# Kernel tuning notes

Measured on AMD Instinct MI355X. Metric: run time of the kernel, lower is better.

Reference implementation:

```python
import jax, jax.numpy as jnp
import numpy as np
from jax import lax

V, E, H = 32000, 512, 512
B, S = 64, 64


def _lstm_cell(x, h, c, wih, whh, b):
    # PyTorch gate order: i, f, g, o
    g = x @ wih.T + h @ whh.T + b
    i, f, gg, o = jnp.split(g, 4, axis=-1)
    c2 = jax.nn.sigmoid(f) * c + jax.nn.sigmoid(i) * jnp.tanh(gg)
    h2 = jax.nn.sigmoid(o) * jnp.tanh(c2)
    return h2, c2


def setup_inputs() -> dict:
    key = jax.random.key(0)
    ks = jax.random.split(key, 16)
    s = 0.05
    return {
        "hidden_state": jax.random.normal(ks[0], (4, B, H), jnp.float32) * s,
        "cell_state": jax.random.normal(ks[1], (4, B, H), jnp.float32) * s,
        "Y": jax.random.randint(ks[2], (B, S), 0, V),
        "emb": jax.random.normal(ks[3], (V, E), jnp.float32) * s,
        "w_ih_l0": jax.random.normal(ks[4], (2, 4 * H, E), jnp.float32) * s,
        "w_hh_l0": jax.random.normal(ks[5], (2, 4 * H, H), jnp.float32) * s,
        "b_ih_l0": jax.random.normal(ks[6], (2, 4 * H), jnp.float32) * s,
        "b_hh_l0": jax.random.normal(ks[7], (2, 4 * H), jnp.float32) * s,
        "w_ih_l1": jax.random.normal(ks[8], (2, 4 * H, 2 * H), jnp.float32) * s,
        "w_hh_l1": jax.random.normal(ks[9], (2, 4 * H, H), jnp.float32) * s,
        "b_ih_l1": jax.random.normal(ks[10], (2, 4 * H), jnp.float32) * s,
        "b_hh_l1": jax.random.normal(ks[11], (2, 4 * H), jnp.float32) * s,
        "fc_w": jax.random.normal(ks[12], (V, 2 * H), jnp.float32) * s,
        "fc_b": jax.random.normal(ks[13], (V,), jnp.float32) * s,
    }


def reference(hidden_state, cell_state, Y, emb, w_ih_l0, w_hh_l0, b_ih_l0,
              b_hh_l0, w_ih_l1, w_hh_l1, b_ih_l1, b_hh_l1, fc_w, fc_b):
    # Deterministic teacher-forcing: input at step 0 is Y[:,1]; at step i>0 it is Y[:,i-1].
    idx_seq = jnp.concatenate([Y[:, 1:2], Y[:, :-1]], axis=1)  # (B,S)
    xs = idx_seq.T  # (S,B)
    b0 = b_ih_l0 + b_hh_l0  # (2,4H)
    b1 = b_ih_l1 + b_hh_l1

    def step(carry, idx):
        h, c = carry  # (4,B,H): [l0_fwd, l0_bwd, l1_fwd, l1_bwd]
        x = emb[idx]  # (B,E)
        h0f, c0f = _lstm_cell(x, h[0], c[0], w_ih_l0[0], w_hh_l0[0], b0[0])
        h0b, c0b = _lstm_cell(x, h[1], c[1], w_ih_l0[1], w_hh_l0[1], b0[1])
        x1 = jnp.concatenate([h0f, h0b], axis=-1)  # (B,2H)
        h1f, c1f = _lstm_cell(x1, h[2], c[2], w_ih_l1[0], w_hh_l1[0], b1[0])
        h1b, c1b = _lstm_cell(x1, h[3], c[3], w_ih_l1[1], w_hh_l1[1], b1[1])
        out = jnp.concatenate([h1f, h1b], axis=-1)  # (B,2H)
        h2 = jnp.stack([h0f, h0b, h1f, h1b])
        c2 = jnp.stack([c0f, c0b, c1f, c1b])
        return (h2, c2), out

    (_, _), outs = lax.scan(step, (hidden_state, cell_state), xs)  # (S,B,2H)
    logits = outs @ fc_w.T + fc_b  # (S,B,V)
    # permute to (B,S,V) then flatten, as in the torch code
    return jnp.transpose(logits, (1, 0, 2)).reshape(-1, fc_w.shape[0])
```

## Files before the change

### kernel.cpp

```cpp
#include <hip/hip_runtime.h>
#include <hip/hip_bf16.h>
#include <stdint.h>

#define S_ 64
#define B_ 64
#define E_ 512
#define H_ 512
#define V_ 32000
#define G4 2048
#define SB 4096
#define NG 4096

typedef __attribute__((ext_vector_type(8))) short short8;
typedef __attribute__((ext_vector_type(4))) float f32x4;
typedef __attribute__((ext_vector_type(4))) int i32x4;

static __device__ __forceinline__ unsigned short f2bf(float f) {
  unsigned u = __float_as_uint(f);
  u += 0x7fff + ((u >> 16) & 1);
  return (unsigned short)(u >> 16);
}
static __device__ __forceinline__ float sigm(float x) {
  return 1.f / (1.f + expf(-x));
}

__device__ __forceinline__ void gload_lds16(const void* g, void* l) {
  __builtin_amdgcn_global_load_lds(
      (const __attribute__((address_space(1))) void*)g,
      (__attribute__((address_space(3))) void*)l, 16, 0, 0);
}

__device__ __forceinline__ void st128_sys(void* p, i32x4 v) {
  asm volatile("global_store_dwordx4 %0, %1, off sc0 sc1"
               :: "v"((unsigned long long)p), "v"(v) : "memory");
}
__device__ __forceinline__ void wait_vm0() {
  asm volatile("s_waitcnt vmcnt(0)" ::: "memory");
}

__device__ __forceinline__ void spin_ge(unsigned* c, unsigned tgt) {
  while (__hip_atomic_load(c, __ATOMIC_RELAXED, __HIP_MEMORY_SCOPE_AGENT) < tgt)
    __builtin_amdgcn_s_sleep(1);
}
__device__ __forceinline__ void arrive(unsigned* c) {
  __hip_atomic_fetch_add(c, 1u, __ATOMIC_RELAXED, __HIP_MEMORY_SCOPE_AGENT);
}

#define CIDX(t, d, p) ((((t) * 8) + ((d) * 4) + (p)) * 64)
#define CNT_BYTES (64 * 8 * 64 * 4)

__global__ void k_f2bf(const float* __restrict__ in, unsigned short* __restrict__ out, int n) {
  int i = blockIdx.x * blockDim.x + threadIdx.x;
  int stride = gridDim.x * blockDim.x;
  for (; i < n; i += stride) out[i] = f2bf(in[i]);
}

__global__ void k_addbias(const float* __restrict__ a, const float* __restrict__ b,
                          float* __restrict__ out, int n) {
  int i = blockIdx.x * blockDim.x + threadIdx.x;
  if (i < n) out[i] = a[i] + b[i];
}

__global__ void k_gather(const int* __restrict__ Y, const float* __restrict__ emb,
                         unsigned short* __restrict__ X) {
  int sb = blockIdx.x;
  int t = sb >> 6, b = sb & 63;
  int idx = (t == 0) ? Y[b * S_ + 1] : Y[b * S_ + t - 1];
  const float* src = emb + (size_t)idx * E_;
  unsigned short* dst = X + (size_t)sb * E_;
  for (int e = threadIdx.x; e < E_; e += blockDim.x) dst[e] = f2bf(src[e]);
}

__global__ void k_init_h(const float* __restrict__ hid,
                         unsigned short* __restrict__ h0i, unsigned short* __restrict__ h1i) {
  int i = blockIdx.x * blockDim.x + threadIdx.x;
  if (i >= 4 * B_ * H_) return;
  unsigned short v = f2bf(hid[i]);
  if (i < 2 * B_ * H_) h0i[i] = v;
  else h1i[i - 2 * B_ * H_] = v;
}

template <bool PERMUTE, bool NT>
__global__ __launch_bounds__(256) void k_gemm_nt(
    const unsigned short* __restrict__ A, const unsigned short* __restrict__ B,
    const float* __restrict__ bias, float* __restrict__ C,
    int M, int N, int K, int nTM, int nwg) {
  __shared__ unsigned short Als[128 * 32];
  __shared__ unsigned short Bls[128 * 32];
  int tid = threadIdx.x;
  int o = blockIdx.x;
  int wg = (o & 7) * (nwg >> 3) + (o >> 3);
  int bm = wg % nTM, bn = wg / nTM;
  int w = tid >> 6, l = tid & 63;
  int wr = w >> 1, wc = w & 1;
  int lr = l & 15, hi = l >> 4;
  int c0 = w * 128 + l;
  int row0 = c0 >> 2, ks0 = (((c0 & 3) ^ (row0 & 3)) * 8);
  int c1 = c0 + 64;
  int row1 = c1 >> 2, ks1 = (((c1 & 3) ^ (row1 & 3)) * 8);
  const unsigned short* Ab = A + (size_t)(bm * 128) * K;
  const unsigned short* Bb = B + (size_t)(bn * 128) * K;
  unsigned short* AlsW = &Als[w * 1024];
  unsigned short* BlsW = &Bls[w * 1024];
  int co = ((hi ^ (lr & 3)) * 8);
  f32x4 acc[4][4] = {};
  for (int kk = 0; kk < K; kk += 32) {
    __syncthreads();
    gload_lds16(Ab + (size_t)row0 * K + kk + ks0, AlsW);
    gload_lds16(Ab + (size_t)row1 * K + kk + ks1, AlsW + 512);
    gload_lds16(Bb + (size_t)row0 * K + kk + ks0, BlsW);
    gload_lds16(Bb + (size_t)row1 * K + kk + ks1, BlsW + 512);
    __syncthreads();
    short8 af[4], bfr[4];
#pragma unroll
    for (int r = 0; r < 4; r++)
      af[r] = *(const short8*)&Als[(wr * 64 + r * 16 + lr) * 32 + co];
#pragma unroll
    for (int c4 = 0; c4 < 4; c4++)
      bfr[c4] = *(const short8*)&Bls[(wc * 64 + c4 * 16 + lr) * 32 + co];
#pragma unroll
    for (int r = 0; r < 4; r++)
#pragma unroll
      for (int c4 = 0; c4 < 4; c4++)
        acc[r][c4] = __builtin_amdgcn_mfma_f32_16x16x32_bf16(af[r], bfr[c4], acc[r][c4], 0, 0, 0);
  }
  int rbase = bm * 128 + wr * 64 + hi * 4;
  int cbase = bn * 128 + wc * 64 + lr;
#pragma unroll
  for (int r = 0; r < 4; r++) {
#pragma unroll
    for (int c4 = 0; c4 < 4; c4++) {
      int cc = cbase + c4 * 16;
      float bv = bias[cc];
#pragma unroll
      for (int j = 0; j < 4; j++) {
        int rr = rbase + r * 16 + j;
        size_t orow = PERMUTE ? (size_t)((rr & 63) * 64 + (rr >> 6)) : (size_t)rr;
        float v = acc[r][c4][j] + bv;
        float* p = &C[orow * (size_t)N + cc];
        if (NT) __builtin_nontemporal_store(v, p);
        else *p = v;
      }
    }
  }
}

#define LDW0 520
#define LDW1 1544
#define NBLK 192

__global__ __launch_bounds__(256) void k_fused_lstm(
    const unsigned short* __restrict__ h0i,
    const unsigned short* __restrict__ h1i,
    const float* __restrict__ cell,
    const unsigned short* __restrict__ whh0,
    const unsigned short* __restrict__ wih1,
    const unsigned short* __restrict__ whh1,
    const float* __restrict__ b1s,
    const float* __restrict__ G0,
    unsigned short* __restrict__ H0,
    unsigned short* __restrict__ O1,
    unsigned* __restrict__ cnt0, unsigned* __restrict__ cnt1) {
  __shared__ unsigned short SM[32 * LDW1];
  __shared__ __align__(16) unsigned short HS[64 * 16];
  int tid = threadIdx.x;
  int w = tid >> 6, l = tid & 63;
  int lr = l & 15, hi = l >> 4;

  if (blockIdx.x < 64) {
    int d = blockIdx.x >> 5, jt = blockIdx.x & 31;
    const unsigned short* Wd = whh0 + (size_t)d * (G4 * H_);
    for (int c = tid; c < 64 * 64; c += 256) {
      int row = c >> 6, ck = c & 63;
      int g = row >> 4, r16 = row & 15;
      *(int4*)&SM[row * LDW0 + ck * 8] =
          *(const int4*)&Wd[(size_t)(g * H_ + jt * 16 + r16) * H_ + ck * 8];
    }
    int j = jt * 16 + lr;
    int b0 = w * 16 + hi * 4;
    f32x4 creg;
    {
      const float* cd = cell + (size_t)d * (B_ * H_);
#pragma unroll
      for (int jj = 0; jj < 4; jj++) creg[jj] = cd[(size_t)(b0 + jj) * H_ + j];
    }
    __syncthreads();
    const float* G_dj = G0 + d * G4;
    float gv[4][4];
    auto preloadG = [&](int t) {
#pragma unroll
      for (int jj = 0; jj < 4; jj++) {
        const float* Gb = G_dj + (size_t)(t * B_ + b0 + jj) * NG;
#pragma unroll
        for (int g = 0; g < 4; g++) gv[g][jj] = Gb[g * 512 + j];
      }
    };
    preloadG(0);
    for (int t = 0; t < S_; ++t) {
      if (t >= 1) {
        if (tid < 4) spin_ge(&cnt0[CIDX(t - 1, d, tid)], 8);
        __syncthreads();
      }
      const unsigned short* hp = (t == 0) ? h0i + (size_t)d * (B_ * H_)
                                          : H0 + (size_t)(t - 1) * B_ * 1024 + d * 512;
      size_t hstr = (t == 0) ? (size_t)H_ : 1024;
      const unsigned short* arow = hp + (size_t)(w * 16 + lr) * hstr + hi * 8;
      f32x4 acc[4] = {};
#pragma unroll
      for (int ki = 0; ki < 16; ki++) {
        short8 a = *(const short8*)&arow[ki * 32];
#pragma unroll
        for (int g = 0; g < 4; g++) {
          short8 bfr = *(const short8*)&SM[(g * 16 + lr) * LDW0 + ki * 32 + hi * 8];
          acc[g] = __builtin_amdgcn_mfma_f32_16x16x32_bf16(a, bfr, acc[g], 0, 0, 0);
        }
      }
#pragma unroll
      for (int jj = 0; jj < 4; jj++) {
        float gi = acc[0][jj] + gv[0][jj];
        float gf = acc[1][jj] + gv[1][jj];
        float gg = acc[2][jj] + gv[2][jj];
        float go = acc[3][jj] + gv[3][jj];
        float c = sigm(gf) * creg[jj] + sigm(gi) * tanhf(gg);
        creg[jj] = c;
        HS[(b0 + jj) * 16 + lr] = f2bf(sigm(go) * tanhf(c));
      }
      __syncthreads();
      unsigned short* Ho = H0 + (size_t)t * B_ * 1024 + d * 512 + jt * 16;
      if (tid < 128) {
        int r = tid >> 1, half = tid & 1;
        i32x4 v = *(const i32x4*)&HS[r * 16 + half * 8];
        st128_sys(&Ho[(size_t)r * 1024 + half * 8], v);
      }
      wait_vm0();
      __syncthreads();
      if (tid == 0) arrive(&cnt0[CIDX(t, d, jt & 3)]);
      if (t + 1 < S_) preloadG(t + 1);
    }
  } else {
    int idx = blockIdx.x - 64;
    int d = idx >> 6, jt8 = idx & 63;
    int j0 = jt8 * 8;
    {
      const unsigned short* Wih = wih1 + (size_t)d * (G4 * 1024);
      const unsigned short* Whh = whh1 + (size_t)d * (G4 * H_);
      for (int c = tid; c < 32 * 192; c += 256) {
        int r = c / 192, ck = c - r * 192;
        int g = r >> 3, jc = r & 7;
        const unsigned short* src =
            (ck < 128) ? Wih + (size_t)(g * H_ + j0 + jc) * 1024 + ck * 8
                       : Whh + (size_t)(g * H_ + j0 + jc) * H_ + (ck - 128) * 8;
        *(int4*)&SM[r * LDW1 + ck * 8] = *(const int4*)src;
      }
    }
    int j = j0 + (lr & 7);
    const float* b1d = b1s + d * G4;
    float bi_ = b1d[j], bf_ = b1d[512 + j], bg_ = b1d[1024 + j], bo_ = b1d[1536 + j];
    int b0 = w * 16 + hi * 4;
    f32x4 creg = {};
    if (lr < 8) {
      const float* cd = cell + (size_t)(2 + d) * (B_ * H_);
#pragma unroll
      for (int jj = 0; jj < 4; jj++) creg[jj] = cd[(size_t)(b0 + jj) * H_ + j];
    }
    __syncthreads();

    f32x4 acc0, acc1;
    {
      if (tid < 8) spin_ge(&cnt0[CIDX(0, 0, 0) + tid * 64], 8);
      __syncthreads();
      acc0 = {}; acc1 = {};
      const unsigned short* x1row = H0 + ((size_t)0 * B_ + w * 16 + lr) * 1024 + hi * 8;
#pragma unroll 8
      for (int ki = 0; ki < 32; ki++) {
        short8 a = *(const short8*)&x1row[ki * 32];
        short8 bA = *(const short8*)&SM[(size_t)lr * LDW1 + ki * 32 + hi * 8];
        short8 bB = *(const short8*)&SM[(size_t)(16 + lr) * LDW1 + ki * 32 + hi * 8];
        acc0 = __builtin_amdgcn_mfma_f32_16x16x32_bf16(a, bA, acc0, 0, 0, 0);
        acc1 = __builtin_amdgcn_mfma_f32_16x16x32_bf16(a, bB, acc1, 0, 0, 0);
      }
    }
    for (int t = 0; t < S_; ++t) {
      if (t >= 1) {
        if (tid < 4) spin_ge(&cnt1[CIDX(t - 1, d, tid)], 16);
        __syncthreads();
      }
      const unsigned short* hprev = (t == 0)
          ? h1i + (size_t)d * (B_ * H_) + (size_t)(w * 16 + lr) * H_ + hi * 8
          : O1 + ((size_t)(t - 1) * B_ + w * 16 + lr) * 1024 + d * 512 + hi * 8;
#pragma unroll 8
      for (int ki = 0; ki < 16; ki++) {
        short8 a = *(const short8*)&hprev[ki * 32];
        short8 bA = *(const short8*)&SM[(size_t)lr * LDW1 + 1024 + ki * 32 + hi * 8];
        short8 bB = *(const short8*)&SM[(size_t)(16 + lr) * LDW1 + 1024 + ki * 32 + hi * 8];
        acc0 = __builtin_amdgcn_mfma_f32_16x16x32_bf16(a, bA, acc0, 0, 0, 0);
        acc1 = __builtin_amdgcn_mfma_f32_16x16x32_bf16(a, bB, acc1, 0, 0, 0);
      }
      float pf[4], po[4];
#pragma unroll
      for (int jj = 0; jj < 4; jj++) {
        pf[jj] = __shfl_xor(acc0[jj], 8);
        po[jj] = __shfl_xor(acc1[jj], 8);
      }
      if (lr < 8) {
#pragma unroll
        for (int jj = 0; jj < 4; jj++) {
          float gi = acc0[jj] + bi_;
          float gf = pf[jj] + bf_;
          float gg = acc1[jj] + bg_;
          float go = po[jj] + bo_;
          float c = sigm(gf) * creg[jj] + sigm(gi) * tanhf(gg);
          creg[jj] = c;
          HS[(b0 + jj) * 8 + lr] = f2bf(sigm(go) * tanhf(c));
        }
      }
      __syncthreads();
      unsigned short* Oo = O1 + (size_t)t * B_ * 1024 + d * 512 + j0;
      if (tid < 64) {
        i32x4 v = *(const i32x4*)&HS[tid * 8];
        st128_sys(&Oo[(size_t)tid * 1024], v);
      }
      wait_vm0();
      __syncthreads();
      if (tid == 0 && t + 1 < S_) arrive(&cnt1[CIDX(t, d, jt8 & 3)]);
      if (t + 1 < S_) {
        if (tid < 8) spin_ge(&cnt0[CIDX(t + 1, 0, 0) + tid * 64], 8);
        __syncthreads();
        acc0 = {}; acc1 = {};
        const unsigned short* x1row =
            H0 + ((size_t)(t + 1) * B_ + w * 16 + lr) * 1024 + hi * 8;
#pragma unroll 8
        for (int ki = 0; ki < 32; ki++) {
          short8 a = *(const short8*)&x1row[ki * 32];
          short8 bA = *(const short8*)&SM[(size_t)lr * LDW1 + ki * 32 + hi * 8];
          short8 bB = *(const short8*)&SM[(size_t)(16 + lr) * LDW1 + ki * 32 + hi * 8];
          acc0 = __builtin_amdgcn_mfma_f32_16x16x32_bf16(a, bA, acc0, 0, 0, 0);
          acc1 = __builtin_amdgcn_mfma_f32_16x16x32_bf16(a, bB, acc1, 0, 0, 0);
        }
      }
    }
  }
}

extern "C" void kernel_launch(void* const* d_in, const int* in_sizes, int n_in,
                              void* d_out, int out_size, void* d_ws, size_t ws_size,
                              hipStream_t stream) {
  const float* hidden = (const float*)d_in[0];
  const float* cell   = (const float*)d_in[1];
  const int*   Y      = (const int*)d_in[2];
  const float* emb    = (const float*)d_in[3];
  const float* wih0   = (const float*)d_in[4];
  const float* whh0   = (const float*)d_in[5];
  const float* bih0   = (const float*)d_in[6];
  const float* bhh0   = (const float*)d_in[7];
  const float* wih1   = (const float*)d_in[8];
  const float* whh1   = (const float*)d_in[9];
  const float* bih1   = (const float*)d_in[10];
  const float* bhh1   = (const float*)d_in[11];
  const float* fcw    = (const float*)d_in[12];
  const float* fcb    = (const float*)d_in[13];

  char* ws = (char*)d_ws;
  size_t off = 0;
  auto alloc = [&](size_t bytes) {
    void* p = ws + off;
    off += (bytes + 255) & ~(size_t)255;
    return p;
  };
  unsigned short* wih0b = (unsigned short*)alloc((size_t)2 * G4 * E_ * 2);
  unsigned short* whh0b = (unsigned short*)alloc((size_t)2 * G4 * H_ * 2);
  unsigned short* wih1b = (unsigned short*)alloc((size_t)2 * G4 * 1024 * 2);
  unsigned short* whh1b = (unsigned short*)alloc((size_t)2 * G4 * H_ * 2);
  unsigned short* fcwb  = (unsigned short*)alloc((size_t)V_ * 1024 * 2);
  unsigned short* Xb    = (unsigned short*)alloc((size_t)SB * E_ * 2);
  unsigned short* H0    = (unsigned short*)alloc((size_t)SB * 1024 * 2);
  unsigned short* O1    = (unsigned short*)alloc((size_t)SB * 1024 * 2);
  unsigned short* h0i   = (unsigned short*)alloc((size_t)2 * B_ * H_ * 2);
  unsigned short* h1i   = (unsigned short*)alloc((size_t)2 * B_ * H_ * 2);
  float* b0s = (float*)alloc((size_t)2 * G4 * 4);
  float* b1s = (float*)alloc((size_t)2 * G4 * 4);
  unsigned* cnt0 = (unsigned*)alloc(CNT_BYTES);
  unsigned* cnt1 = (unsigned*)alloc(CNT_BYTES);
  (void)ws_size;

  float* G0 = (float*)d_out;

  k_f2bf<<<2048, 256, 0, stream>>>(wih0, wih0b, 2 * G4 * E_);
  k_f2bf<<<2048, 256, 0, stream>>>(whh0, whh0b, 2 * G4 * H_);
  k_f2bf<<<2048, 256, 0, stream>>>(wih1, wih1b, 2 * G4 * 1024);
  k_f2bf<<<2048, 256, 0, stream>>>(whh1, whh1b, 2 * G4 * H_);
  k_f2bf<<<4096, 256, 0, stream>>>(fcw, fcwb, V_ * 1024);
  k_addbias<<<16, 256, 0, stream>>>(bih0, bhh0, b0s, 2 * G4);
  k_addbias<<<16, 256, 0, stream>>>(bih1, bhh1, b1s, 2 * G4);
  k_gather<<<SB, 256, 0, stream>>>(Y, emb, Xb);
  k_init_h<<<512, 256, 0, stream>>>(hidden, h0i, h1i);
  (void)hipMemsetAsync(cnt0, 0, CNT_BYTES, stream);
  (void)hipMemsetAsync(cnt1, 0, CNT_BYTES, stream);

  k_gemm_nt<false, false><<<(SB / 128) * (NG / 128), 256, 0, stream>>>(
      Xb, wih0b, b0s, G0, SB, NG, E_, SB / 128, (SB / 128) * (NG / 128));

  k_fused_lstm<<<NBLK, 256, 0, stream>>>(h0i, h1i, cell, whh0b, wih1b, whh1b,
                                         b1s, G0, H0, O1, cnt0, cnt1);

  k_gemm_nt<true, true><<<(SB / 128) * (V_ / 128), 256, 0, stream>>>(
      O1, fcwb, fcb, (float*)d_out, SB, V_, 1024, SB / 128, (SB / 128) * (V_ / 128));
}
```

Baseline: 1.205 ms.

## Fuse FC projection into persistent LSTM kernel, overlapping with recurrence

```diff
diff --git a/kernel.cpp b/kernel.cpp
--- a/kernel.cpp
+++ b/kernel.cpp
@@ -9,7 +9,9 @@
 #define V_ 32000
 #define G4 2048
 #define SB 4096
-#define NG 4096
+
+#define OROW_US 64000
+#define GTAIL_US 59904
 
 typedef __attribute__((ext_vector_type(8))) short short8;
 typedef __attribute__((ext_vector_type(4))) float f32x4;
@@ -20,6 +22,9 @@
   u += 0x7fff + ((u >> 16) & 1);
   return (unsigned short)(u >> 16);
 }
+static __device__ __forceinline__ float bf2f(unsigned short u) {
+  return __uint_as_float((unsigned)u << 16);
+}
 static __device__ __forceinline__ float sigm(float x) {
   return 1.f / (1.f + expf(-x));
 }
@@ -41,6 +46,10 @@
 __device__ __forceinline__ void spin_ge(unsigned* c, unsigned tgt) {
   while (__hip_atomic_load(c, __ATOMIC_RELAXED, __HIP_MEMORY_SCOPE_AGENT) < tgt)
     __builtin_amdgcn_s_sleep(1);
+}
+__device__ __forceinline__ void spin_ge_slow(unsigned* c, unsigned tgt) {
+  while (__hip_atomic_load(c, __ATOMIC_RELAXED, __HIP_MEMORY_SCOPE_AGENT) < tgt)
+    __builtin_amdgcn_s_sleep(16);
 }
 __device__ __forceinline__ void arrive(unsigned* c) {
   __hip_atomic_fetch_add(c, 1u, __ATOMIC_RELAXED, __HIP_MEMORY_SCOPE_AGENT);
@@ -80,11 +89,10 @@
   else h1i[i - 2 * B_ * H_] = v;
 }
 
-template <bool PERMUTE, bool NT>
-__global__ __launch_bounds__(256) void k_gemm_nt(
+__global__ __launch_bounds__(256) void k_gemm_g0(
     const unsigned short* __restrict__ A, const unsigned short* __restrict__ B,
-    const float* __restrict__ bias, float* __restrict__ C,
-    int M, int N, int K, int nTM, int nwg) {
+    const float* __restrict__ bias, unsigned short* __restrict__ C,
+    int K, int nTM, int nwg) {
   __shared__ unsigned short Als[128 * 32];
   __shared__ unsigned short Bls[128 * 32];
   int tid = threadIdx.x;
@@ -135,11 +143,7 @@
 #pragma unroll
       for (int j = 0; j < 4; j++) {
         int rr = rbase + r * 16 + j;
-        size_t orow = PERMUTE ? (size_t)((rr & 63) * 64 + (rr >> 6)) : (size_t)rr;
-        float v = acc[r][c4][j] + bv;
-        float* p = &C[orow * (size_t)N + cc];
-        if (NT) __builtin_nontemporal_store(v, p);
-        else *p = v;
+        C[(size_t)rr * OROW_US + GTAIL_US + cc] = f2bf(acc[r][c4][j] + bv);
       }
     }
   }
@@ -147,9 +151,8 @@
 
 #define LDW0 520
 #define LDW1 1544
-#define NBLK 192
-
-__global__ __launch_bounds__(256) void k_fused_lstm(
+
+__global__ __launch_bounds__(256) void k_mega(
     const unsigned short* __restrict__ h0i,
     const unsigned short* __restrict__ h1i,
     const float* __restrict__ cell,
@@ -157,7 +160,9 @@
     const unsigned short* __restrict__ wih1,
     const unsigned short* __restrict__ whh1,
     const float* __restrict__ b1s,
-    const float* __restrict__ G0,
+    float* __restrict__ dout,
+    const unsigned short* __restrict__ fcwb,
+    const float* __restrict__ fcb,
     unsigned short* __restrict__ H0,
     unsigned short* __restrict__ O1,
     unsigned* __restrict__ cnt0, unsigned* __restrict__ cnt1) {
@@ -166,6 +171,7 @@
   int tid = threadIdx.x;
   int w = tid >> 6, l = tid & 63;
   int lr = l & 15, hi = l >> 4;
+  const unsigned short* G0u = (const unsigned short*)dout;
 
   if (blockIdx.x < 64) {
     int d = blockIdx.x >> 5, jt = blockIdx.x & 31;
@@ -185,14 +191,14 @@
       for (int jj = 0; jj < 4; jj++) creg[jj] = cd[(size_t)(b0 + jj) * H_ + j];
     }
     __syncthreads();
-    const float* G_dj = G0 + d * G4;
     float gv[4][4];
     auto preloadG = [&](int t) {
 #pragma unroll
       for (int jj = 0; jj < 4; jj++) {
-        const float* Gb = G_dj + (size_t)(t * B_ + b0 + jj) * NG;
-#pragma unroll
-        for (int g = 0; g < 4; g++) gv[g][jj] = Gb[g * 512 + j];
+        const unsigned short* Gb =
+            G0u + (size_t)(t * B_ + b0 + jj) * OROW_US + GTAIL_US + d * 2048 + j;
+#pragma unroll
+        for (int g = 0; g < 4; g++) gv[g][jj] = bf2f(Gb[g * 512]);
       }
     };
     preloadG(0);
@@ -237,7 +243,7 @@
       if (tid == 0) arrive(&cnt0[CIDX(t, d, jt & 3)]);
       if (t + 1 < S_) preloadG(t + 1);
     }
-  } else {
+  } else if (blockIdx.x < 192) {
     int idx = blockIdx.x - 64;
     int d = idx >> 6, jt8 = idx & 63;
     int j0 = jt8 * 8;
@@ -322,7 +328,7 @@
       }
       wait_vm0();
       __syncthreads();
-      if (tid == 0 && t + 1 < S_) arrive(&cnt1[CIDX(t, d, jt8 & 3)]);
+      if (tid == 0) arrive(&cnt1[CIDX(t, d, jt8 & 3)]);
       if (t + 1 < S_) {
         if (tid < 8) spin_ge(&cnt0[CIDX(t + 1, 0, 0) + tid * 64], 8);
         __syncthreads();
@@ -339,6 +345,70 @@
         }
       }
     }
+  } else {
+    int i = blockIdx.x - 192;
+    unsigned short* Als = SM;
+    unsigned short* Bls = SM + 4096;
+    int wr = w >> 1, wc = w & 1;
+    int c0 = w * 128 + l;
+    int row0 = c0 >> 2, ks0 = (((c0 & 3) ^ (row0 & 3)) * 8);
+    int c1 = c0 + 64;
+    int row1 = c1 >> 2, ks1 = (((c1 & 3) ^ (row1 & 3)) * 8);
+    int co = ((hi ^ (lr & 3)) * 8);
+    auto tile = [&](int bm, int bn) {
+      const unsigned short* Ab = O1 + (size_t)(bm * 128) * 1024;
+      const unsigned short* Bb = fcwb + (size_t)(bn * 128) * 1024;
+      unsigned short* AlsW = &Als[w * 1024];
+      unsigned short* BlsW = &Bls[w * 1024];
+      f32x4 acc[4][4] = {};
+      for (int kk = 0; kk < 1024; kk += 32) {
+        __syncthreads();
+        gload_lds16(Ab + (size_t)row0 * 1024 + kk + ks0, AlsW);
+        gload_lds16(Ab + (size_t)row1 * 1024 + kk + ks1, AlsW + 512);
+        gload_lds16(Bb + (size_t)row0 * 1024 + kk + ks0, BlsW);
+        gload_lds16(Bb + (size_t)row1 * 1024 + kk + ks1, BlsW + 512);
+        __syncthreads();
+        short8 af[4], bfr[4];
+#pragma unroll
+        for (int r = 0; r < 4; r++)
+          af[r] = *(const short8*)&Als[(wr * 64 + r * 16 + lr) * 32 + co];
+#pragma unroll
+        for (int c4 = 0; c4 < 4; c4++)
+          bfr[c4] = *(const short8*)&Bls[(wc * 64 + c4 * 16 + lr) * 32 + co];
+#pragma unroll
+        for (int r = 0; r < 4; r++)
+#pragma unroll
+          for (int c4 = 0; c4 < 4; c4++)
+            acc[r][c4] = __builtin_amdgcn_mfma_f32_16x16x32_bf16(af[r], bfr[c4], acc[r][c4], 0, 0, 0);
+      }
+      int rbase = bm * 128 + wr * 64 + hi * 4;
+      int cbase = bn * 128 + wc * 64 + lr;
+#pragma unroll
+      for (int r = 0; r < 4; r++) {
+#pragma unroll
+        for (int c4 = 0; c4 < 4; c4++) {
+          int cc = cbase + c4 * 16;
+          float bv = fcb[cc];
+#pragma unroll
+          for (int j = 0; j < 4; j++) {
+            int rr = rbase + r * 16 + j;
+            size_t orow = (size_t)((rr & 63) * 64 + (rr >> 6));
+            __builtin_nontemporal_store(acc[r][c4][j] + bv, &dout[orow * V_ + cc]);
+          }
+        }
+      }
+    };
+    for (int bm = 0; bm < 32; ++bm) {
+      if (tid < 16) {
+        int t = bm * 2 + (tid >> 3), dd = (tid >> 2) & 1, p = tid & 3;
+        spin_ge_slow(&cnt1[CIDX(t, dd, p)], 16);
+      }
+      __syncthreads();
+      for (int bn = i; bn < 234; bn += 64) tile(bm, bn);
+    }
+    if (tid < 8) spin_ge_slow(&cnt1[CIDX(63, tid >> 2, tid & 3)], 16);
+    __syncthreads();
+    for (int k = i; k < 512; k += 64) tile(k >> 4, 234 + (k & 15));
   }
 }
 
@@ -383,8 +453,6 @@
   unsigned* cnt1 = (unsigned*)alloc(CNT_BYTES);
   (void)ws_size;
 
-  float* G0 = (float*)d_out;
-
   k_f2bf<<<2048, 256, 0, stream>>>(wih0, wih0b, 2 * G4 * E_);
   k_f2bf<<<2048, 256, 0, stream>>>(whh0, whh0b, 2 * G4 * H_);
   k_f2bf<<<2048, 256, 0, stream>>>(wih1, wih1b, 2 * G4 * 1024);
@@ -397,12 +465,9 @@
   (void)hipMemsetAsync(cnt0, 0, CNT_BYTES, stream);
   (void)hipMemsetAsync(cnt1, 0, CNT_BYTES, stream);
 
-  k_gemm_nt<false, false><<<(SB / 128) * (NG / 128), 256, 0, stream>>>(
-      Xb, wih0b, b0s, G0, SB, NG, E_, SB / 128, (SB / 128) * (NG / 128));
-
-  k_fused_lstm<<<NBLK, 256, 0, stream>>>(h0i, h1i, cell, whh0b, wih1b, whh1b,
-                                         b1s, G0, H0, O1, cnt0, cnt1);
-
-  k_gemm_nt<true, true><<<(SB / 128) * (V_ / 128), 256, 0, stream>>>(
-      O1, fcwb, fcb, (float*)d_out, SB, V_, 1024, SB / 128, (SB / 128) * (V_ / 128));
-}
+  k_gemm_g0<<<1024, 256, 0, stream>>>(Xb, wih0b, b0s, (unsigned short*)d_out,
+                                      E_, SB / 128, 1024);
+
+  k_mega<<<256, 256, 0, stream>>>(h0i, h1i, cell, whh0b, wih1b, whh1b, b1s,
+                                  (float*)d_out, fcwb, fcb, H0, O1, cnt0, cnt1);
+}
```

After: 2.527 ms. 2.1x slower.
